# Optimization experiments

Measured on AMD Instinct MI355X. Metric: run time of the kernel, lower is better.

The kernel has to match this reference:

```python
import jax, jax.numpy as jnp
import numpy as np
from jax import lax

B, T, H = 2, 1024, 2048
NH, D = 8, 128          # heads, head_dim
P = NH * D              # projection size
K = 4                   # short conv kernel size
EPS = 1e-6
SCALE = D ** -0.5


def _causal_conv_silu(x, w):
    # x: (B,T,C); w: (C,K) depthwise causal conv followed by silu (ShortConvolution)
    C = w.shape[0]
    kern = jnp.transpose(w)[:, None, :]  # (K,1,C)
    y = lax.conv_general_dilated(x, kern, window_strides=(1,), padding=[(K - 1, 0)],
                                 dimension_numbers=('NWC', 'WIO', 'NWC'),
                                 feature_group_count=C)
    return jax.nn.silu(y)


def _l2norm(x):
    return x * jax.lax.rsqrt(jnp.sum(x * x, axis=-1, keepdims=True) + EPS)


def _forward(hidden_states, Wq, Wk, Wv, conv_q, conv_k, conv_v, A_log, dt_bias,
             Wfa, Wfb, Wb, Wga, Wgb, norm_weight, Wo):
    x = hidden_states                                # (B,T,H)
    q = _causal_conv_silu(x @ Wq.T, conv_q)          # (B,T,P)
    k = _causal_conv_silu(x @ Wk.T, conv_k)
    v = _causal_conv_silu(x @ Wv.T, conv_v)
    # fused_kda_gate: g = -exp(A_log) * softplus(f_b(f_a(x)) + dt_bias), per (h,d) channel
    gf = (x @ Wfa.T) @ Wfb.T                         # (B,T,P) low-rank gate proj
    gf = gf.reshape(B, T, NH, D) + dt_bias.reshape(NH, D)
    g = -jnp.exp(A_log)[None, None, :, None] * jax.nn.softplus(gf)  # (B,T,NH,D) log-decay <= 0
    beta = jax.nn.sigmoid(x @ Wb.T)                  # (B,T,NH)
    q = _l2norm(q.reshape(B, T, NH, D)) * SCALE      # use_qk_l2norm_in_kernel + 1/sqrt(d) scale
    k = _l2norm(k.reshape(B, T, NH, D))
    v = v.reshape(B, T, NH, D)

    # gated delta-rule recurrence (KDA): per-key-channel decay, beta-weighted delta update
    def step(S, inp):
        q_t, k_t, v_t, g_t, b_t = inp                # (B,NH,D), beta (B,NH)
        S = S * jnp.exp(g_t)[..., None]              # decay rows (key dim) of S[.,.,dk,dv]
        kv = jnp.einsum('bhk,bhkv->bhv', k_t, S)
        delta = (v_t - kv) * b_t[..., None]
        S = S + jnp.einsum('bhk,bhv->bhkv', k_t, delta)
        o_t = jnp.einsum('bhk,bhkv->bhv', q_t, S)
        return S, o_t

    tfirst = lambda a: jnp.moveaxis(a, 1, 0)         # time-major for scan
    S0 = jnp.zeros((B, NH, D, D), x.dtype)
    _, o = lax.scan(step, S0, (tfirst(q), tfirst(k), tfirst(v), tfirst(g), tfirst(beta)))
    o = jnp.moveaxis(o, 0, 1)                        # (B,T,NH,D)

    # FusedRMSNormGated(sigmoid): gate applied before RMS normalization (Mamba2 convention)
    gate = ((x @ Wga.T) @ Wgb.T).reshape(B, T, NH, D)
    og = o * jax.nn.sigmoid(gate)
    og = og * jax.lax.rsqrt(jnp.mean(og * og, axis=-1, keepdims=True) + EPS) * norm_weight
    return og.reshape(B * T, P) @ Wo.T               # (B*T, H)


def setup_inputs():
    ks = jax.random.split(jax.random.key(0), 16)
    s = 0.02
    f32 = jnp.float32
    return {
        'hidden_states': jax.random.normal(ks[0], (B, T, H), f32),
        'Wq': jax.random.normal(ks[1], (P, H), f32) * s,
        'Wk': jax.random.normal(ks[2], (P, H), f32) * s,
        'Wv': jax.random.normal(ks[3], (P, H), f32) * s,
        'conv_q': jax.random.normal(ks[4], (P, K), f32) * 0.3,
        'conv_k': jax.random.normal(ks[5], (P, K), f32) * 0.3,
        'conv_v': jax.random.normal(ks[6], (P, K), f32) * 0.3,
        'A_log': jnp.log(jax.random.uniform(ks[7], (NH,), f32, 1.0, 16.0)),
        'dt_bias': jax.random.normal(ks[8], (P,), f32) * 0.5,
        'Wfa': jax.random.normal(ks[9], (D, H), f32) * s,
        'Wfb': jax.random.normal(ks[10], (P, D), f32) * s,
        'Wb': jax.random.normal(ks[11], (NH, H), f32) * s,
        'Wga': jax.random.normal(ks[12], (D, H), f32) * s,
        'Wgb': jax.random.normal(ks[13], (P, D), f32) * s,
        'norm_weight': jnp.ones((D,), f32),
        'Wo': jax.random.normal(ks[14], (H, P), f32) * s,
    }


def reference(hidden_states, Wq, Wk, Wv, conv_q, conv_k, conv_v, A_log, dt_bias,
              Wfa, Wfb, Wb, Wga, Wgb, norm_weight, Wo):
    return _forward(hidden_states, Wq, Wk, Wv, conv_q, conv_k, conv_v, A_log, dt_bias,
                    Wfa, Wfb, Wb, Wga, Wgb, norm_weight, Wo)
```

## Files before the change

### kernel.cpp

```cpp
#include <hip/hip_runtime.h>
#include <hip/hip_bf16.h>
#include <cstddef>
#include <cstdint>

#define Bb 2
#define Tt 1024
#define Hh 2048
#define NHh 8
#define Dd 128
#define Pp (NHh * Dd)
#define NW (5 * Pp)
#define Kk 4
#define EPSf 1e-6f
#define SCALEf 0.08838834764831845f
#define DVQ 16
#define CHUNK 8

typedef short bf16x8 __attribute__((ext_vector_type(8)));
typedef float f32x4 __attribute__((ext_vector_type(4)));
typedef float f32x2 __attribute__((ext_vector_type(2)));

template <int CTRL>
__device__ __forceinline__ float dpp_add(float x) {
  int yi = __builtin_amdgcn_update_dpp(0, __builtin_bit_cast(int, x), CTRL, 0xF, 0xF, true);
  return x + __builtin_bit_cast(float, yi);
}
__device__ __forceinline__ float row16_sum(float x) {
  x = dpp_add<0xB1>(x);
  x = dpp_add<0x4E>(x);
  x = dpp_add<0x124>(x);
  x = dpp_add<0x128>(x);
  return x;
}

__device__ __forceinline__ void gload_lds16(const void* g, void* l) {
  __builtin_amdgcn_global_load_lds((const __attribute__((address_space(1))) void*)g,
                                   (__attribute__((address_space(3))) void*)l, 16, 0, 0);
}

__global__ __launch_bounds__(256) void cvt_bf16(const float* __restrict__ src,
                                                __hip_bfloat16* __restrict__ dst, int n) {
  const int i = (blockIdx.x * 256 + threadIdx.x) * 8;
  if (i >= n) return;
  const float4 a = *reinterpret_cast<const float4*>(src + i);
  const float4 b = *reinterpret_cast<const float4*>(src + i + 4);
  __hip_bfloat16 t[8];
  t[0] = __float2bfloat16(a.x); t[1] = __float2bfloat16(a.y);
  t[2] = __float2bfloat16(a.z); t[3] = __float2bfloat16(a.w);
  t[4] = __float2bfloat16(b.x); t[5] = __float2bfloat16(b.y);
  t[6] = __float2bfloat16(b.z); t[7] = __float2bfloat16(b.w);
  *reinterpret_cast<uint4*>(dst + i) = *reinterpret_cast<const uint4*>(t);
}

__global__ __launch_bounds__(256) void cvt_bf16_x4(const float* __restrict__ s0,
                                                   const float* __restrict__ s1,
                                                   const float* __restrict__ s2,
                                                   const float* __restrict__ s3,
                                                   __hip_bfloat16* __restrict__ d0,
                                                   __hip_bfloat16* __restrict__ d1,
                                                   __hip_bfloat16* __restrict__ d2,
                                                   __hip_bfloat16* __restrict__ d3,
                                                   int nper) {
  const int bpa = nper / 2048;
  const int a = blockIdx.x / bpa;
  const int i = (blockIdx.x % bpa) * 2048 + threadIdx.x * 8;
  const float* src = (a == 0) ? s0 : (a == 1) ? s1 : (a == 2) ? s2 : s3;
  __hip_bfloat16* dst = (a == 0) ? d0 : (a == 1) ? d1 : (a == 2) ? d2 : d3;
  const float4 x = *reinterpret_cast<const float4*>(src + i);
  const float4 y = *reinterpret_cast<const float4*>(src + i + 4);
  __hip_bfloat16 t[8];
  t[0] = __float2bfloat16(x.x); t[1] = __float2bfloat16(x.y);
  t[2] = __float2bfloat16(x.z); t[3] = __float2bfloat16(x.w);
  t[4] = __float2bfloat16(y.x); t[5] = __float2bfloat16(y.y);
  t[6] = __float2bfloat16(y.z); t[7] = __float2bfloat16(y.w);
  *reinterpret_cast<uint4*>(dst + i) = *reinterpret_cast<const uint4*>(t);
}

__global__ __launch_bounds__(256) void gemm_nn_bf16(const float* __restrict__ A,
                                                    const float* __restrict__ B,
                                                    __hip_bfloat16* __restrict__ Cbf,
                                                    int M, int N, int K) {
  __shared__ float As[64][33];
  __shared__ float Bs[32][65];
  const int bm = blockIdx.y * 64, bn = blockIdx.x * 64;
  const int tid = threadIdx.x;
  const int tx = tid & 15, ty = tid >> 4;
  float acc[4][4];
#pragma unroll
  for (int i = 0; i < 4; i++)
#pragma unroll
    for (int j = 0; j < 4; j++) acc[i][j] = 0.f;
  for (int k0 = 0; k0 < K; k0 += 32) {
#pragma unroll
    for (int i = 0; i < 8; i++) {
      const int idx = tid + i * 256;
      const int r = idx >> 5, c = idx & 31;
      As[r][c] = A[(size_t)(bm + r) * K + k0 + c];
    }
#pragma unroll
    for (int i = 0; i < 8; i++) {
      const int idx = tid + i * 256;
      const int r = idx >> 6, c = idx & 63;
      Bs[r][c] = B[(size_t)(k0 + r) * N + bn + c];
    }
    __syncthreads();
#pragma unroll
    for (int kk = 0; kk < 32; kk++) {
      float a[4], b[4];
#pragma unroll
      for (int i = 0; i < 4; i++) a[i] = As[ty * 4 + i][kk];
#pragma unroll
      for (int j = 0; j < 4; j++) b[j] = Bs[kk][tx * 4 + j];
#pragma unroll
      for (int i = 0; i < 4; i++)
#pragma unroll
        for (int j = 0; j < 4; j++) acc[i][j] += a[i] * b[j];
    }
    __syncthreads();
  }
#pragma unroll
  for (int i = 0; i < 4; i++) {
    const int row = bm + ty * 4 + i;
#pragma unroll
    for (int j = 0; j < 4; j++) {
      const int col = bn + tx * 4 + j;
      Cbf[(size_t)row * N + col] = __float2bfloat16(acc[i][j]);
    }
  }
}

__global__ __launch_bounds__(256) void gemm_bf16_lds(const __hip_bfloat16* __restrict__ A,
                                                     const __hip_bfloat16* __restrict__ B,
                                                     float* __restrict__ C,
                                                     __hip_bfloat16* __restrict__ Cbf,
                                                     int M, int N, int K, int outmode) {
  __shared__ __align__(16) __hip_bfloat16 As[128 * 64];
  __shared__ __align__(16) __hip_bfloat16 Bs[128 * 64];
  const int tid = threadIdx.x;
  const int wave = tid >> 6;
  const int lane = tid & 63;
  const int wm = (wave >> 1) * 64;
  const int wn = (wave & 1) * 64;
  const int bm = blockIdx.y * 128;
  const int bn = blockIdx.x * 128;
  const int l15 = lane & 15;
  const int l4 = lane >> 4;
  const int srow = lane >> 3;
  const int scol = (lane & 7) * 8;

  f32x4 acc[4][4];
#pragma unroll
  for (int i = 0; i < 4; i++)
#pragma unroll
    for (int j = 0; j < 4; j++) acc[i][j] = (f32x4){0.f, 0.f, 0.f, 0.f};

  for (int k0 = 0; k0 < K; k0 += 64) {
#pragma unroll
    for (int i = 0; i < 4; i++) {
      const int s = wave * 4 + i;
      const int row = s * 8 + srow;
      gload_lds16(A + (size_t)(bm + row) * K + k0 + scol, &As[s * 512]);
      gload_lds16(B + (size_t)(bn + row) * K + k0 + scol, &Bs[s * 512]);
    }
    __syncthreads();
    bf16x8 af[4][2], bfv[4][2];
#pragma unroll
    for (int kf = 0; kf < 2; kf++) {
      const int kc = kf * 32 + l4 * 8;
#pragma unroll
      for (int mf = 0; mf < 4; mf++)
        af[mf][kf] = *reinterpret_cast<const bf16x8*>(&As[(wm + mf * 16 + l15) * 64 + kc]);
#pragma unroll
      for (int nf = 0; nf < 4; nf++)
        bfv[nf][kf] = *reinterpret_cast<const bf16x8*>(&Bs[(wn + nf * 16 + l15) * 64 + kc]);
    }
#pragma unroll
    for (int kf = 0; kf < 2; kf++)
#pragma unroll
      for (int mf = 0; mf < 4; mf++)
#pragma unroll
        for (int nf = 0; nf < 4; nf++)
          acc[mf][nf] = __builtin_amdgcn_mfma_f32_16x16x32_bf16(af[mf][kf], bfv[nf][kf],
                                                                acc[mf][nf], 0, 0, 0);
    __syncthreads();
  }
#pragma unroll
  for (int mf = 0; mf < 4; mf++) {
#pragma unroll
    for (int nf = 0; nf < 4; nf++) {
      const int col = bn + wn + nf * 16 + l15;
#pragma unroll
      for (int r = 0; r < 4; r++) {
        const int row = bm + wm + mf * 16 + l4 * 4 + r;
        if (outmode == 0) C[(size_t)row * N + col] = acc[mf][nf][r];
        else Cbf[(size_t)row * N + col] = __float2bfloat16(acc[mf][nf][r]);
      }
    }
  }
}

__global__ __launch_bounds__(256) void gemm_nt(const float* __restrict__ A,
                                               const float* __restrict__ Bm,
                                               float* __restrict__ C,
                                               int M, int N, int Kd) {
  __shared__ float As[16][64];
  __shared__ float Bs[16][64];
  const int bm = blockIdx.y * 64;
  const int bn = blockIdx.x * 64;
  const int tid = threadIdx.x;
  const int tx = tid & 15;
  const int ty = tid >> 4;
  const int lr = tid >> 2;
  const int lc = (tid & 3) << 2;
  float acc[4][4];
#pragma unroll
  for (int i = 0; i < 4; i++)
#pragma unroll
    for (int j = 0; j < 4; j++) acc[i][j] = 0.f;
  for (int k0 = 0; k0 < Kd; k0 += 16) {
    float4 a4 = make_float4(0.f, 0.f, 0.f, 0.f);
    float4 b4 = make_float4(0.f, 0.f, 0.f, 0.f);
    const int ar = bm + lr;
    if (ar < M) a4 = *reinterpret_cast<const float4*>(A + (size_t)ar * Kd + k0 + lc);
    const int br = bn + lr;
    if (br < N) b4 = *reinterpret_cast<const float4*>(Bm + (size_t)br * Kd + k0 + lc);
    As[lc + 0][lr] = a4.x; As[lc + 1][lr] = a4.y; As[lc + 2][lr] = a4.z; As[lc + 3][lr] = a4.w;
    Bs[lc + 0][lr] = b4.x; Bs[lc + 1][lr] = b4.y; Bs[lc + 2][lr] = b4.z; Bs[lc + 3][lr] = b4.w;
    __syncthreads();
#pragma unroll
    for (int kk = 0; kk < 16; kk++) {
      float4 av = *reinterpret_cast<const float4*>(&As[kk][ty << 2]);
      float4 bv = *reinterpret_cast<const float4*>(&Bs[kk][tx << 2]);
      float a[4] = {av.x, av.y, av.z, av.w};
      float b[4] = {bv.x, bv.y, bv.z, bv.w};
#pragma unroll
      for (int i = 0; i < 4; i++)
#pragma unroll
        for (int j = 0; j < 4; j++) acc[i][j] += a[i] * b[j];
    }
    __syncthreads();
  }
#pragma unroll
  for (int i = 0; i < 4; i++) {
    const int row = bm + (ty << 2) + i;
    if (row >= M) continue;
#pragma unroll
    for (int j = 0; j < 4; j++) {
      const int col = bn + (tx << 2) + j;
      if (col < N) C[(size_t)row * N + col] = acc[i][j];
    }
  }
}

__global__ __launch_bounds__(256) void beta_kernel(const float* __restrict__ x,
                                                   const float* __restrict__ Wb,
                                                   float* __restrict__ beta) {
  __shared__ float xs[Hh];
  const int m = blockIdx.x;
  const int tid = threadIdx.x;
  for (int i = tid; i < Hh; i += 256) xs[i] = x[(size_t)m * Hh + i];
  __syncthreads();
  const int h = tid >> 5;
  const int lane = tid & 31;
  float acc = 0.f;
  for (int i = lane; i < Hh; i += 32) acc += xs[i] * Wb[(size_t)h * Hh + i];
#pragma unroll
  for (int o = 16; o > 0; o >>= 1) acc += __shfl_down(acc, o, 32);
  if (lane == 0) beta[(size_t)m * NHh + h] = 1.f / (1.f + expf(-acc));
}

__global__ __launch_bounds__(256) void g_kernel(const float* __restrict__ src,
                                                int sstride, int scol,
                                                float* __restrict__ dst,
                                                const float* __restrict__ dtb,
                                                const float* __restrict__ A_log) {
  const size_t i = (size_t)blockIdx.x * 256 + threadIdx.x;
  const int c = (int)(i % Pp);
  const size_t row = i / Pp;
  const int h = c / Dd;
  const float xv = src[row * sstride + scol + c] + dtb[c];
  const float sp = (xv > 20.f) ? xv : log1pf(expf(xv));
  dst[i] = expf(-expf(A_log[h]) * sp);
}

__global__ __launch_bounds__(128) void conv_silu_norm(const float* __restrict__ xin,
                                                      const float* __restrict__ w,
                                                      float* __restrict__ out,
                                                      int mode, int instride, int coff) {
  const int idx = blockIdx.x;
  const int h = idx % NHh;
  const int bt = idx / NHh;
  const int t = bt % Tt;
  const int d = threadIdx.x;
  const int c = h * Dd + d;
  float acc = 0.f;
#pragma unroll
  for (int j = 0; j < Kk; j++) {
    const int tt = t - (Kk - 1) + j;
    float xv = 0.f;
    if (tt >= 0) xv = xin[(size_t)(bt - (Kk - 1) + j) * instride + coff + c];
    acc += w[c * Kk + j] * xv;
  }
  float y = acc / (1.f + expf(-acc));
  float r = y;
  if (mode > 0) {
    float ss = y * y;
#pragma unroll
    for (int o = 32; o > 0; o >>= 1) ss += __shfl_down(ss, o);
    __shared__ float red[2];
    if ((d & 63) == 0) red[d >> 6] = ss;
    __syncthreads();
    const float tot = red[0] + red[1];
    const float inv = rsqrtf(tot + EPSf);
    r = y * inv * (mode == 2 ? SCALEf : 1.f);
  }
  out[(size_t)bt * Pp + c] = r;
}

__global__ __launch_bounds__(128) void conv3b_kernel(const float* __restrict__ qkvpre,
                                                     const float* __restrict__ cq,
                                                     const float* __restrict__ ck,
                                                     const float* __restrict__ cv,
                                                     float* __restrict__ outbase,
                                                     int instride) {
  const int nper = (Bb * Tt / 4) * NHh;
  const int which = blockIdx.x / nper;
  const int idx = blockIdx.x % nper;
  const float* w = (which == 0) ? cq : (which == 1) ? ck : cv;
  const int mode = (which == 0) ? 2 : (which == 1) ? 1 : 0;
  const int h = idx % NHh;
  const int bt0 = (idx / NHh) * 4;
  const int t0 = bt0 % Tt;
  const int d = threadIdx.x;
  const int c = h * Dd + d;

  float xw[7];
#pragma unroll
  for (int i = 0; i < 7; i++) {
    const int tt = t0 - 3 + i;
    xw[i] = (tt >= 0) ? qkvpre[(size_t)(bt0 - 3 + i) * instride + which * Pp + c] : 0.f;
  }
  const float w0 = w[c * Kk + 0], w1 = w[c * Kk + 1], w2 = w[c * Kk + 2], w3 = w[c * Kk + 3];
  float y[4];
#pragma unroll
  for (int jj = 0; jj < 4; jj++) {
    const float a = w0 * xw[jj] + w1 * xw[jj + 1] + w2 * xw[jj + 2] + w3 * xw[jj + 3];
    y[jj] = a / (1.f + expf(-a));
  }
  if (mode > 0) {
    float ss[4];
#pragma unroll
    for (int jj = 0; jj < 4; jj++) ss[jj] = y[jj] * y[jj];
#pragma unroll
    for (int o = 32; o > 0; o >>= 1) {
#pragma unroll
      for (int jj = 0; jj < 4; jj++) ss[jj] += __shfl_down(ss[jj], o);
    }
    __shared__ float red[2][4];
    if ((d & 63) == 0) {
#pragma unroll
      for (int jj = 0; jj < 4; jj++) red[d >> 6][jj] = ss[jj];
    }
    __syncthreads();
    const float sc = (mode == 2) ? SCALEf : 1.f;
#pragma unroll
    for (int jj = 0; jj < 4; jj++)
      y[jj] = y[jj] * rsqrtf(red[0][jj] + red[1][jj] + EPSf) * sc;
  }
  float* outp = outbase + (size_t)which * (Bb * Tt) * Pp;
#pragma unroll
  for (int jj = 0; jj < 4; jj++) outp[(size_t)(bt0 + jj) * Pp + c] = y[jj];
}

__global__ __launch_bounds__(128) void scan_kernel(const float* __restrict__ q,
                                                   const float* __restrict__ k,
                                                   const float* __restrict__ v,
                                                   const float* __restrict__ eg,
                                                   const float* __restrict__ beta,
                                                   float* __restrict__ o) {
  const int blk = blockIdx.x;
  const int bh = blk & 15;
  const int dvq = blk >> 4;
  const int b = bh >> 3, h = bh & 7;
  const int tid = threadIdx.x;
  const int qr = tid & 15;
  const int dvl = tid >> 4;
  const int dv = dvq * 8 + dvl;

  __shared__ __align__(16) float qs[2][CHUNK][16][12];
  __shared__ __align__(16) float ks[2][CHUNK][16][12];
  __shared__ __align__(16) float legs[2][CHUNK][16][12];
  __shared__ float vs[2][CHUNK][8];
  __shared__ float betas[2][CHUNK];

  f32x2 s2[4];
#pragma unroll
  for (int i = 0; i < 4; i++) s2[i] = (f32x2){0.f, 0.f};

  const size_t base = (size_t)(b * Tt) * Pp + h * Dd;
  const int le = tid;

  float rq[CHUNK], rk[CHUNK], re[CHUNK], rv[CHUNK], rb = 0.f;
  auto load_chunk = [&](int t0) {
    const size_t coff = base + (size_t)t0 * Pp;
#pragma unroll
    for (int j = 0; j < CHUNK; j++) {
      rq[j] = q[coff + (size_t)j * Pp + le];
      rk[j] = k[coff + (size_t)j * Pp + le];
      re[j] = eg[coff + (size_t)j * Pp + le];
    }
    if (tid < 8) {
#pragma unroll
      for (int j = 0; j < CHUNK; j++) rv[j] = v[coff + (size_t)j * Pp + dvq * 8 + tid];
    } else if (tid < 8 + CHUNK) {
      rb = beta[(size_t)(b * Tt + t0 + tid - 8) * NHh + h];
    }
  };
  auto write_lds = [&](int bufw) {
#pragma unroll
    for (int j = 0; j < CHUNK; j++) {
      qs[bufw][j][le >> 3][le & 7] = rq[j];
      ks[bufw][j][le >> 3][le & 7] = rk[j];
      legs[bufw][j][le >> 3][le & 7] = re[j];
    }
    if (tid < 8) {
#pragma unroll
      for (int j = 0; j < CHUNK; j++) vs[bufw][j][tid] = rv[j];
    } else if (tid < 8 + CHUNK) {
      betas[bufw][tid - 8] = rb;
    }
  };
  auto unpack = [](const float4& a, const float4& b, f32x2 out[4]) {
    out[0] = (f32x2){a.x, a.y}; out[1] = (f32x2){a.z, a.w};
    out[2] = (f32x2){b.x, b.y}; out[3] = (f32x2){b.z, b.w};
  };

  load_chunk(0);
  write_lds(0);
  __syncthreads();
  const int NC = Tt / CHUNK;
  size_t off = base;
  for (int c = 0; c < NC; c++) {
    if (c + 1 < NC) load_chunk((c + 1) * CHUNK);
    const int buf = c & 1;
    float vv[CHUNK], bb[CHUNK], opart[CHUNK];
#pragma unroll
    for (int j = 0; j < CHUNK; j++) { vv[j] = vs[buf][j][dvl]; bb[j] = betas[buf][j]; }

    f32x2 ck2[4], ce2[4], cq2[4], kt2[4];
    {
      const float4 k0 = *reinterpret_cast<const float4*>(&ks[buf][0][qr][0]);
      const float4 k1 = *reinterpret_cast<const float4*>(&ks[buf][0][qr][4]);
      const float4 e0 = *reinterpret_cast<const float4*>(&legs[buf][0][qr][0]);
      const float4 e1 = *reinterpret_cast<const float4*>(&legs[buf][0][qr][4]);
      const float4 q0 = *reinterpret_cast<const float4*>(&qs[buf][0][qr][0]);
      const float4 q1 = *reinterpret_cast<const float4*>(&qs[buf][0][qr][4]);
      unpack(k0, k1, ck2); unpack(e0, e1, ce2); unpack(q0, q1, cq2);
#pragma unroll
      for (int i = 0; i < 4; i++) kt2[i] = ck2[i] * ce2[i];
    }

#pragma unroll
    for (int j = 0; j < CHUNK; j++) {
      float4 nk0, nk1, ne0, ne1, nq0, nq1;
      if (j + 1 < CHUNK) {
        nk0 = *reinterpret_cast<const float4*>(&ks[buf][j + 1][qr][0]);
        nk1 = *reinterpret_cast<const float4*>(&ks[buf][j + 1][qr][4]);
        ne0 = *reinterpret_cast<const float4*>(&legs[buf][j + 1][qr][0]);
        ne1 = *reinterpret_cast<const float4*>(&legs[buf][j + 1][qr][4]);
        nq0 = *reinterpret_cast<const float4*>(&qs[buf][j + 1][qr][0]);
        nq1 = *reinterpret_cast<const float4*>(&qs[buf][j + 1][qr][4]);
      }
      f32x2 es0 = ce2[0] * s2[0], es1 = ce2[1] * s2[1];
      f32x2 es2v = ce2[2] * s2[2], es3 = ce2[3] * s2[3];
      f32x2 kva = kt2[0] * s2[0];
      f32x2 kvb = kt2[1] * s2[1];
      kva = kt2[2] * s2[2] + kva;
      kvb = kt2[3] * s2[3] + kvb;
      kva = kva + kvb;
      const float kvp = row16_sum(kva.x + kva.y);
      const float delta = (vv[j] - kvp) * bb[j];
      const f32x2 d2 = (f32x2){delta, delta};
      f32x2 o2;
      s2[0] = ck2[0] * d2 + es0;  o2 = cq2[0] * s2[0];
      s2[1] = ck2[1] * d2 + es1;  o2 = cq2[1] * s2[1] + o2;
      s2[2] = ck2[2] * d2 + es2v; o2 = cq2[2] * s2[2] + o2;
      s2[3] = ck2[3] * d2 + es3;  o2 = cq2[3] * s2[3] + o2;
      opart[j] = o2.x + o2.y;
      if (j + 1 < CHUNK) {
        unpack(nk0, nk1, ck2); unpack(ne0, ne1, ce2); unpack(nq0, nq1, cq2);
#pragma unroll
        for (int i = 0; i < 4; i++) kt2[i] = ck2[i] * ce2[i];
      }
    }
#pragma unroll
    for (int j = 0; j < CHUNK; j++) opart[j] = row16_sum(opart[j]);
    if (qr == 0) {
#pragma unroll
      for (int j = 0; j < CHUNK; j++) o[off + (size_t)j * Pp + dv] = opart[j];
    }
    if (c + 1 < NC) write_lds(buf ^ 1);
    __syncthreads();
    off += (size_t)CHUNK * Pp;
  }
}

__global__ __launch_bounds__(128) void gated_norm(float* __restrict__ o,
                                                  const float* __restrict__ gate,
                                                  int gstride,
                                                  const float* __restrict__ nw,
                                                  __hip_bfloat16* __restrict__ ogbf) {
  const int idx = blockIdx.x;
  const int h = idx % NHh;
  const int bt = idx / NHh;
  const int d = threadIdx.x;
  const size_t off = (size_t)bt * Pp + h * Dd;
  const float ov = o[off + d];
  const float gt = gate[(size_t)bt * gstride + h * Dd + d];
  const float val = ov / (1.f + expf(-gt));
  float ss = val * val;
#pragma unroll
  for (int sh = 32; sh > 0; sh >>= 1) ss += __shfl_down(ss, sh);
  __shared__ float red[2];
  if ((d & 63) == 0) red[d >> 6] = ss;
  __syncthreads();
  const float mean = (red[0] + red[1]) * (1.f / Dd);
  const float res = val * rsqrtf(mean + EPSf) * nw[d];
  if (ogbf != nullptr) ogbf[off + d] = __float2bfloat16(res);
  else o[off + d] = res;
}

extern "C" void kernel_launch(void* const* d_in, const int* in_sizes, int n_in,
                              void* d_out, int out_size, void* d_ws, size_t ws_size,
                              hipStream_t stream) {
  const float* x     = (const float*)d_in[0];
  const float* Wq    = (const float*)d_in[1];
  const float* Wk    = (const float*)d_in[2];
  const float* Wv    = (const float*)d_in[3];
  const float* cq    = (const float*)d_in[4];
  const float* ck    = (const float*)d_in[5];
  const float* cv    = (const float*)d_in[6];
  const float* A_log = (const float*)d_in[7];
  const float* dtb   = (const float*)d_in[8];
  const float* Wfa   = (const float*)d_in[9];
  const float* Wfb   = (const float*)d_in[10];
  const float* Wb    = (const float*)d_in[11];
  const float* Wga   = (const float*)d_in[12];
  const float* Wgb   = (const float*)d_in[13];
  const float* nw    = (const float*)d_in[14];
  const float* Wo    = (const float*)d_in[15];
  float* outp = (float*)d_out;

  const int M = Bb * Tt;
  const size_t MP = (size_t)M * Pp;
  float* ws = (float*)d_ws;
  float* qkvpre = ws;
  float* qb   = qkvpre + (size_t)M * NW;
  float* kb   = qb + MP;
  float* vb   = kb + MP;
  float* gbuf = vb + MP;
  float* obuf = gbuf + MP;
  float* betab = obuf + MP;
  float* gfa  = betab + (size_t)M * NHh;
  float* gga  = gfa + (size_t)M * Dd;
  float* f32end = gga + (size_t)M * Dd;

  __hip_bfloat16* xhi    = (__hip_bfloat16*)f32end;
  __hip_bfloat16* Wqkvbf = xhi + (size_t)M * Hh;
  __hip_bfloat16* Wobf   = Wqkvbf + (size_t)NW * Hh;
  __hip_bfloat16* end    = Wobf + (size_t)Hh * Pp;
  __hip_bfloat16* ogbf   = (__hip_bfloat16*)qb;
  const bool use_mfma = ws_size >= (size_t)((char*)end - (char*)d_ws);

  const dim3 blk(256);
  if (use_mfma) {
    cvt_bf16<<<(int)((size_t)M * Hh / 2048), blk, 0, stream>>>(x, xhi, M * Hh);
    cvt_bf16_x4<<<4 * (int)((size_t)Pp * Hh / 2048), blk, 0, stream>>>(
        Wq, Wk, Wv, Wo, Wqkvbf, Wqkvbf + (size_t)Pp * Hh, Wqkvbf + (size_t)2 * Pp * Hh,
        Wobf, Pp * Hh);
    gemm_nn_bf16<<<dim3(Hh / 64, Pp / 64), blk, 0, stream>>>(Wgb, Wga,
                                                             Wqkvbf + (size_t)3 * Pp * Hh,
                                                             Pp, Hh, Dd);
    gemm_nn_bf16<<<dim3(Hh / 64, Pp / 64), blk, 0, stream>>>(Wfb, Wfa,
                                                             Wqkvbf + (size_t)4 * Pp * Hh,
                                                             Pp, Hh, Dd);
    gemm_bf16_lds<<<dim3(NW / 128, M / 128), blk, 0, stream>>>(xhi, Wqkvbf, qkvpre, nullptr,
                                                               M, NW, Hh, 0);
    g_kernel<<<(int)(MP / 256), blk, 0, stream>>>(qkvpre, NW, 4 * Pp, gbuf, dtb, A_log);
    beta_kernel<<<M, 256, 0, stream>>>(x, Wb, betab);
    conv3b_kernel<<<3 * (M / 4) * NHh, 128, 0, stream>>>(qkvpre, cq, ck, cv, qb, NW);
    scan_kernel<<<Bb * NHh * DVQ, 128, 0, stream>>>(qb, kb, vb, gbuf, betab, obuf);
    gated_norm<<<M * NHh, 128, 0, stream>>>(obuf, qkvpre + (size_t)3 * Pp, NW, nw, ogbf);
    gemm_bf16_lds<<<dim3(Hh / 128, M / 128), blk, 0, stream>>>(ogbf, Wobf, outp, nullptr,
                                                               M, Hh, Pp, 0);
  } else {
    float* qpre = qkvpre;
    float* kpre = qkvpre + MP;
    float* vpre = qkvpre + 2 * MP;
    float* gate = qkvpre + 3 * MP;
    gemm_nt<<<dim3(Pp / 64, M / 64), blk, 0, stream>>>(x, Wq, qpre, M, Pp, Hh);
    gemm_nt<<<dim3(Pp / 64, M / 64), blk, 0, stream>>>(x, Wk, kpre, M, Pp, Hh);
    gemm_nt<<<dim3(Pp / 64, M / 64), blk, 0, stream>>>(x, Wv, vpre, M, Pp, Hh);
    gemm_nt<<<dim3(Dd / 64, M / 64), blk, 0, stream>>>(x, Wfa, gfa, M, Dd, Hh);
    gemm_nt<<<dim3(Dd / 64, M / 64), blk, 0, stream>>>(x, Wga, gga, M, Dd, Hh);
    gemm_nt<<<dim3(Pp / 64, M / 64), blk, 0, stream>>>(gfa, Wfb, gbuf, M, Pp, Dd);
    gemm_nt<<<dim3(Pp / 64, M / 64), blk, 0, stream>>>(gga, Wgb, gate, M, Pp, Dd);
    beta_kernel<<<M, 256, 0, stream>>>(x, Wb, betab);
    g_kernel<<<(int)(MP / 256), blk, 0, stream>>>(gbuf, Pp, 0, gbuf, dtb, A_log);
    conv_silu_norm<<<M * NHh, 128, 0, stream>>>(qpre, cq, qb, 2, Pp, 0);
    conv_silu_norm<<<M * NHh, 128, 0, stream>>>(kpre, ck, kb, 1, Pp, 0);
    conv_silu_norm<<<M * NHh, 128, 0, stream>>>(vpre, cv, vb, 0, Pp, 0);
    scan_kernel<<<Bb * NHh * DVQ, 128, 0, stream>>>(qb, kb, vb, gbuf, betab, obuf);
    gated_norm<<<M * NHh, 128, 0, stream>>>(obuf, gate, Pp, nw, nullptr);
    gemm_nt<<<dim3(Hh / 64, M / 64), blk, 0, stream>>>(obuf, Wo, outp, M, Hh, Pp);
  }
}
```

Baseline: 411.6 us.

## Interleave both batch recurrences in one scan block for ILP

Each scan block now runs the recurrences for both batch elements of one head and value slice, interleaving two independent dependency chains. The chunk length drops from 8 to 4 so LDS and register use stay similar, and the grid is halved. The aim is to hide the serial latency of the DPP reductions and FMAs by overlapping two chains. The cost is fewer blocks in flight (128 on a many-CU GPU), more register pressure, and twice as many chunk-loop iterations with their syncs.

Result: slower. 543.1 us (+32.0%).

```diff
diff --git a/kernel.cpp b/kernel.cpp
--- a/kernel.cpp
+++ b/kernel.cpp
@@ -14,7 +14,7 @@
 #define EPSf 1e-6f
 #define SCALEf 0.08838834764831845f
 #define DVQ 16
-#define CHUNK 8
+#define CH4 4
 
 typedef short bf16x8 __attribute__((ext_vector_type(8)));
 typedef float f32x4 __attribute__((ext_vector_type(4)));
@@ -379,58 +379,72 @@
                                                    const float* __restrict__ beta,
                                                    float* __restrict__ o) {
   const int blk = blockIdx.x;
-  const int bh = blk & 15;
-  const int dvq = blk >> 4;
-  const int b = bh >> 3, h = bh & 7;
+  const int h = blk & 7;
+  const int dvq = blk >> 3;
   const int tid = threadIdx.x;
   const int qr = tid & 15;
   const int dvl = tid >> 4;
   const int dv = dvq * 8 + dvl;
 
-  __shared__ __align__(16) float qs[2][CHUNK][16][12];
-  __shared__ __align__(16) float ks[2][CHUNK][16][12];
-  __shared__ __align__(16) float legs[2][CHUNK][16][12];
-  __shared__ float vs[2][CHUNK][8];
-  __shared__ float betas[2][CHUNK];
-
-  f32x2 s2[4];
-#pragma unroll
-  for (int i = 0; i < 4; i++) s2[i] = (f32x2){0.f, 0.f};
-
-  const size_t base = (size_t)(b * Tt) * Pp + h * Dd;
+  __shared__ __align__(16) float qs[2][2][CH4][16][12];
+  __shared__ __align__(16) float ks[2][2][CH4][16][12];
+  __shared__ __align__(16) float legs[2][2][CH4][16][12];
+  __shared__ float vs[2][2][CH4][8];
+  __shared__ float betas[2][2][CH4];
+
+  f32x2 sA[4], sB[4];
+#pragma unroll
+  for (int i = 0; i < 4; i++) { sA[i] = (f32x2){0.f, 0.f}; sB[i] = (f32x2){0.f, 0.f}; }
+
+  const size_t baseA = (size_t)h * Dd;
+  const size_t baseB = (size_t)Tt * Pp + h * Dd;
   const int le = tid;
 
-  float rq[CHUNK], rk[CHUNK], re[CHUNK], rv[CHUNK], rb = 0.f;
+  float rq[2][CH4], rk[2][CH4], re[2][CH4], rv[2][CH4], rb = 0.f;
   auto load_chunk = [&](int t0) {
-    const size_t coff = base + (size_t)t0 * Pp;
-#pragma unroll
-    for (int j = 0; j < CHUNK; j++) {
-      rq[j] = q[coff + (size_t)j * Pp + le];
-      rk[j] = k[coff + (size_t)j * Pp + le];
-      re[j] = eg[coff + (size_t)j * Pp + le];
+#pragma unroll
+    for (int s = 0; s < 2; s++) {
+      const size_t coff = (s ? baseB : baseA) + (size_t)t0 * Pp;
+#pragma unroll
+      for (int j = 0; j < CH4; j++) {
+        rq[s][j] = q[coff + (size_t)j * Pp + le];
+        rk[s][j] = k[coff + (size_t)j * Pp + le];
+        re[s][j] = eg[coff + (size_t)j * Pp + le];
+      }
     }
     if (tid < 8) {
 #pragma unroll
-      for (int j = 0; j < CHUNK; j++) rv[j] = v[coff + (size_t)j * Pp + dvq * 8 + tid];
-    } else if (tid < 8 + CHUNK) {
-      rb = beta[(size_t)(b * Tt + t0 + tid - 8) * NHh + h];
+      for (int s = 0; s < 2; s++)
+#pragma unroll
+        for (int j = 0; j < CH4; j++)
+          rv[s][j] = v[(s ? baseB : baseA) + (size_t)(t0 + j) * Pp + dvq * 8 + tid];
+    } else if (tid < 16) {
+      const int s = (tid - 8) >> 2;
+      const int j = (tid - 8) & 3;
+      rb = beta[(size_t)(s * Tt + t0 + j) * NHh + h];
     }
   };
   auto write_lds = [&](int bufw) {
 #pragma unroll
-    for (int j = 0; j < CHUNK; j++) {
-      qs[bufw][j][le >> 3][le & 7] = rq[j];
-      ks[bufw][j][le >> 3][le & 7] = rk[j];
-      legs[bufw][j][le >> 3][le & 7] = re[j];
-    }
+    for (int s = 0; s < 2; s++)
+#pragma unroll
+      for (int j = 0; j < CH4; j++) {
+        qs[s][bufw][j][le >> 3][le & 7] = rq[s][j];
+        ks[s][bufw][j][le >> 3][le & 7] = rk[s][j];
+        legs[s][bufw][j][le >> 3][le & 7] = re[s][j];
+      }
     if (tid < 8) {
 #pragma unroll
-      for (int j = 0; j < CHUNK; j++) vs[bufw][j][tid] = rv[j];
-    } else if (tid < 8 + CHUNK) {
-      betas[bufw][tid - 8] = rb;
+      for (int s = 0; s < 2; s++)
+#pragma unroll
+        for (int j = 0; j < CH4; j++) vs[s][bufw][j][tid] = rv[s][j];
+    } else if (tid < 16) {
+      betas[(tid - 8) >> 2][bufw][(tid - 8) & 3] = rb;
     }
   };
-  auto unpack = [](const float4& a, const float4& b, f32x2 out[4]) {
+  auto loadpk = [](const float* p, f32x2 out[4]) {
+    const float4 a = *reinterpret_cast<const float4*>(p);
+    const float4 b = *reinterpret_cast<const float4*>(p + 4);
     out[0] = (f32x2){a.x, a.y}; out[1] = (f32x2){a.z, a.w};
     out[2] = (f32x2){b.x, b.y}; out[3] = (f32x2){b.z, b.w};
   };
@@ -438,70 +452,94 @@
   load_chunk(0);
   write_lds(0);
   __syncthreads();
-  const int NC = Tt / CHUNK;
-  size_t off = base;
+  const int NC = Tt / CH4;
+  size_t offA = baseA, offB = baseB;
   for (int c = 0; c < NC; c++) {
-    if (c + 1 < NC) load_chunk((c + 1) * CHUNK);
+    if (c + 1 < NC) load_chunk((c + 1) * CH4);
     const int buf = c & 1;
-    float vv[CHUNK], bb[CHUNK], opart[CHUNK];
-#pragma unroll
-    for (int j = 0; j < CHUNK; j++) { vv[j] = vs[buf][j][dvl]; bb[j] = betas[buf][j]; }
-
-    f32x2 ck2[4], ce2[4], cq2[4], kt2[4];
-    {
-      const float4 k0 = *reinterpret_cast<const float4*>(&ks[buf][0][qr][0]);
-      const float4 k1 = *reinterpret_cast<const float4*>(&ks[buf][0][qr][4]);
-      const float4 e0 = *reinterpret_cast<const float4*>(&legs[buf][0][qr][0]);
-      const float4 e1 = *reinterpret_cast<const float4*>(&legs[buf][0][qr][4]);
-      const float4 q0 = *reinterpret_cast<const float4*>(&qs[buf][0][qr][0]);
-      const float4 q1 = *reinterpret_cast<const float4*>(&qs[buf][0][qr][4]);
-      unpack(k0, k1, ck2); unpack(e0, e1, ce2); unpack(q0, q1, cq2);
-#pragma unroll
-      for (int i = 0; i < 4; i++) kt2[i] = ck2[i] * ce2[i];
-    }
-
-#pragma unroll
-    for (int j = 0; j < CHUNK; j++) {
-      float4 nk0, nk1, ne0, ne1, nq0, nq1;
-      if (j + 1 < CHUNK) {
-        nk0 = *reinterpret_cast<const float4*>(&ks[buf][j + 1][qr][0]);
-        nk1 = *reinterpret_cast<const float4*>(&ks[buf][j + 1][qr][4]);
-        ne0 = *reinterpret_cast<const float4*>(&legs[buf][j + 1][qr][0]);
-        ne1 = *reinterpret_cast<const float4*>(&legs[buf][j + 1][qr][4]);
-        nq0 = *reinterpret_cast<const float4*>(&qs[buf][j + 1][qr][0]);
-        nq1 = *reinterpret_cast<const float4*>(&qs[buf][j + 1][qr][4]);
+    float vvA[CH4], bbA[CH4], opA[CH4], vvB[CH4], bbB[CH4], opB[CH4];
+#pragma unroll
+    for (int j = 0; j < CH4; j++) {
+      vvA[j] = vs[0][buf][j][dvl]; bbA[j] = betas[0][buf][j];
+      vvB[j] = vs[1][buf][j][dvl]; bbB[j] = betas[1][buf][j];
+    }
+
+    f32x2 ckA[4], ceA[4], cqA[4], ktA[4], ckB[4], ceB[4], cqB[4], ktB[4];
+    loadpk(&ks[0][buf][0][qr][0], ckA);
+    loadpk(&legs[0][buf][0][qr][0], ceA);
+    loadpk(&qs[0][buf][0][qr][0], cqA);
+    loadpk(&ks[1][buf][0][qr][0], ckB);
+    loadpk(&legs[1][buf][0][qr][0], ceB);
+    loadpk(&qs[1][buf][0][qr][0], cqB);
+#pragma unroll
+    for (int i = 0; i < 4; i++) { ktA[i] = ckA[i] * ceA[i]; ktB[i] = ckB[i] * ceB[i]; }
+
+#pragma unroll
+    for (int j = 0; j < CH4; j++) {
+      f32x2 nkA[4], neA[4], nqA[4], nkB[4], neB[4], nqB[4];
+      if (j + 1 < CH4) {
+        loadpk(&ks[0][buf][j + 1][qr][0], nkA);
+        loadpk(&legs[0][buf][j + 1][qr][0], neA);
+        loadpk(&qs[0][buf][j + 1][qr][0], nqA);
+        loadpk(&ks[1][buf][j + 1][qr][0], nkB);
+        loadpk(&legs[1][buf][j + 1][qr][0], neB);
+        loadpk(&qs[1][buf][j + 1][qr][0], nqB);
       }
-      f32x2 es0 = ce2[0] * s2[0], es1 = ce2[1] * s2[1];
-      f32x2 es2v = ce2[2] * s2[2], es3 = ce2[3] * s2[3];
-      f32x2 kva = kt2[0] * s2[0];
-      f32x2 kvb = kt2[1] * s2[1];
-      kva = kt2[2] * s2[2] + kva;
-      kvb = kt2[3] * s2[3] + kvb;
-      kva = kva + kvb;
-      const float kvp = row16_sum(kva.x + kva.y);
-      const float delta = (vv[j] - kvp) * bb[j];
-      const f32x2 d2 = (f32x2){delta, delta};
-      f32x2 o2;
-      s2[0] = ck2[0] * d2 + es0;  o2 = cq2[0] * s2[0];
-      s2[1] = ck2[1] * d2 + es1;  o2 = cq2[1] * s2[1] + o2;
-      s2[2] = ck2[2] * d2 + es2v; o2 = cq2[2] * s2[2] + o2;
-      s2[3] = ck2[3] * d2 + es3;  o2 = cq2[3] * s2[3] + o2;
-      opart[j] = o2.x + o2.y;
-      if (j + 1 < CHUNK) {
-        unpack(nk0, nk1, ck2); unpack(ne0, ne1, ce2); unpack(nq0, nq1, cq2);
-#pragma unroll
-        for (int i = 0; i < 4; i++) kt2[i] = ck2[i] * ce2[i];
+      f32x2 esA0 = ceA[0] * sA[0], esA1 = ceA[1] * sA[1];
+      f32x2 esA2 = ceA[2] * sA[2], esA3 = ceA[3] * sA[3];
+      f32x2 kvaA = ktA[0] * sA[0];
+      f32x2 kvbA = ktA[1] * sA[1];
+      kvaA = ktA[2] * sA[2] + kvaA;
+      kvbA = ktA[3] * sA[3] + kvbA;
+      kvaA = kvaA + kvbA;
+
+      f32x2 esB0 = ceB[0] * sB[0], esB1 = ceB[1] * sB[1];
+      f32x2 esB2 = ceB[2] * sB[2], esB3 = ceB[3] * sB[3];
+      f32x2 kvaB = ktB[0] * sB[0];
+      f32x2 kvbB = ktB[1] * sB[1];
+      kvaB = ktB[2] * sB[2] + kvaB;
+      kvbB = ktB[3] * sB[3] + kvbB;
+      kvaB = kvaB + kvbB;
+
+      const float kvpA = row16_sum(kvaA.x + kvaA.y);
+      const float kvpB = row16_sum(kvaB.x + kvaB.y);
+
+      const float deltaA = (vvA[j] - kvpA) * bbA[j];
+      const float deltaB = (vvB[j] - kvpB) * bbB[j];
+      const f32x2 dA = (f32x2){deltaA, deltaA};
+      const f32x2 dB = (f32x2){deltaB, deltaB};
+      f32x2 oA, oB;
+      sA[0] = ckA[0] * dA + esA0;  oA = cqA[0] * sA[0];
+      sB[0] = ckB[0] * dB + esB0;  oB = cqB[0] * sB[0];
+      sA[1] = ckA[1] * dA + esA1;  oA = cqA[1] * sA[1] + oA;
+      sB[1] = ckB[1] * dB + esB1;  oB = cqB[1] * sB[1] + oB;
+      sA[2] = ckA[2] * dA + esA2;  oA = cqA[2] * sA[2] + oA;
+      sB[2] = ckB[2] * dB + esB2;  oB = cqB[2] * sB[2] + oB;
+      sA[3] = ckA[3] * dA + esA3;  oA = cqA[3] * sA[3] + oA;
+      sB[3] = ckB[3] * dB + esB3;  oB = cqB[3] * sB[3] + oB;
+      opA[j] = oA.x + oA.y;
+      opB[j] = oB.x + oB.y;
+      if (j + 1 < CH4) {
+#pragma unroll
+        for (int i = 0; i < 4; i++) {
+          ckA[i] = nkA[i]; ceA[i] = neA[i]; cqA[i] = nqA[i]; ktA[i] = ckA[i] * ceA[i];
+          ckB[i] = nkB[i]; ceB[i] = neB[i]; cqB[i] = nqB[i]; ktB[i] = ckB[i] * ceB[i];
+        }
       }
     }
 #pragma unroll
-    for (int j = 0; j < CHUNK; j++) opart[j] = row16_sum(opart[j]);
+    for (int j = 0; j < CH4; j++) { opA[j] = row16_sum(opA[j]); opB[j] = row16_sum(opB[j]); }
     if (qr == 0) {
 #pragma unroll
-      for (int j = 0; j < CHUNK; j++) o[off + (size_t)j * Pp + dv] = opart[j];
+      for (int j = 0; j < CH4; j++) {
+        o[offA + (size_t)j * Pp + dv] = opA[j];
+        o[offB + (size_t)j * Pp + dv] = opB[j];
+      }
     }
     if (c + 1 < NC) write_lds(buf ^ 1);
     __syncthreads();
-    off += (size_t)CHUNK * Pp;
+    offA += (size_t)CH4 * Pp;
+    offB += (size_t)CH4 * Pp;
   }
 }
 
@@ -589,7 +627,7 @@
     g_kernel<<<(int)(MP / 256), blk, 0, stream>>>(qkvpre, NW, 4 * Pp, gbuf, dtb, A_log);
     beta_kernel<<<M, 256, 0, stream>>>(x, Wb, betab);
     conv3b_kernel<<<3 * (M / 4) * NHh, 128, 0, stream>>>(qkvpre, cq, ck, cv, qb, NW);
-    scan_kernel<<<Bb * NHh * DVQ, 128, 0, stream>>>(qb, kb, vb, gbuf, betab, obuf);
+    scan_kernel<<<NHh * DVQ, 128, 0, stream>>>(qb, kb, vb, gbuf, betab, obuf);
     gated_norm<<<M * NHh, 128, 0, stream>>>(obuf, qkvpre + (size_t)3 * Pp, NW, nw, ogbf);
     gemm_bf16_lds<<<dim3(Hh / 128, M / 128), blk, 0, stream>>>(ogbf, Wobf, outp, nullptr,
                                                                M, Hh, Pp, 0);
@@ -610,7 +648,7 @@
     conv_silu_norm<<<M * NHh, 128, 0, stream>>>(qpre, cq, qb, 2, Pp, 0);
     conv_silu_norm<<<M * NHh, 128, 0, stream>>>(kpre, ck, kb, 1, Pp, 0);
     conv_silu_norm<<<M * NHh, 128, 0, stream>>>(vpre, cv, vb, 0, Pp, 0);
-    scan_kernel<<<Bb * NHh * DVQ, 128, 0, stream>>>(qb, kb, vb, gbuf, betab, obuf);
+    scan_kernel<<<NHh * DVQ, 128, 0, stream>>>(qb, kb, vb, gbuf, betab, obuf);
     gated_norm<<<M * NHh, 128, 0, stream>>>(obuf, gate, Pp, nw, nullptr);
     gemm_nt<<<dim3(Hh / 64, M / 64), blk, 0, stream>>>(obuf, Wo, outp, M, Hh, Pp);
   }
```
